# Optimization experiments

Hardware: AMD Instinct MI355X
Metric: run time of the kernel (lower is better)

Reference implementation:

```python
import jax, jax.numpy as jnp
import numpy as np

N_NODES = 100000
N_EDGES = 1600000
C = 256            # in_channels == out_channels
NUM_BUNDLES = 64
BUNDLE_DIM = 2
NUM_GRAPHS = 128
BN_EPS = 1e-5


def setup_inputs() -> dict:
    key = jax.random.key(0)
    ks = jax.random.split(key, 12)
    x = jax.random.normal(ks[0], (N_NODES, C), dtype=jnp.float32)
    edge_index = jax.random.randint(ks[1], (2, N_EDGES), 0, N_NODES, dtype=jnp.int64)
    batch = jnp.sort(jax.random.randint(ks[2], (N_NODES,), 0, NUM_GRAPHS, dtype=jnp.int64))
    s = 0.05
    # struct_enc MLP: Linear(C, 2*NB) -> GELU -> Linear(2*NB, NB)
    se_w1 = jax.random.normal(ks[3], (C, 2 * NUM_BUNDLES), dtype=jnp.float32) * s
    se_b1 = jnp.zeros((2 * NUM_BUNDLES,), dtype=jnp.float32)
    se_w2 = jax.random.normal(ks[4], (2 * NUM_BUNDLES, NUM_BUNDLES), dtype=jnp.float32) * s
    se_b2 = jnp.zeros((NUM_BUNDLES,), dtype=jnp.float32)
    # LimConv.lin: Linear(C, C)
    lin_w = jax.random.normal(ks[5], (C, C), dtype=jnp.float32) * s
    lin_b = jnp.zeros((C,), dtype=jnp.float32)
    # BatchNorm1d affine params
    bn_gamma = jnp.ones((C,), dtype=jnp.float32)
    bn_beta = jnp.zeros((C,), dtype=jnp.float32)
    return {"x": x, "edge_index": edge_index, "batch": batch,
            "se_w1": se_w1, "se_b1": se_b1, "se_w2": se_w2, "se_b2": se_b2,
            "lin_w": lin_w, "lin_b": lin_b, "bn_gamma": bn_gamma, "bn_beta": bn_beta}


def _lim_layer(x, batch, se_w1, se_b1, se_w2, se_b2, lin_w, lin_b, bn_gamma, bn_beta):
    n = x.shape[0]
    # vector field: [N, NB, 2, fiber]
    vf = x.reshape(n, NUM_BUNDLES, BUNDLE_DIM, -1)
    # struct_enc MLP -> per-bundle angle (tanh-squashed), euler map to SO(2)
    h1 = jax.nn.gelu(x @ se_w1 + se_b1, approximate=False)
    ang = jnp.tanh(h1 @ se_w2 + se_b2)          # [N, NB]
    c, s = jnp.cos(ang), jnp.sin(ang)
    # R[n,b] = [[c,-s],[s,c]]  -> [N, NB, 2, 2]
    rot = jnp.stack([jnp.stack([c, -s], axis=-1),
                     jnp.stack([s, c], axis=-1)], axis=-2)
    # rotate fibers
    vf = jnp.einsum('nbij,nbjf->nbif', rot, vf)
    h = vf.reshape(n, C) @ lin_w + lin_b
    # global mean pool over graphs, then broadcast back to nodes
    sums = jax.ops.segment_sum(h, batch, num_segments=NUM_GRAPHS)
    cnts = jax.ops.segment_sum(jnp.ones((n,), h.dtype), batch, num_segments=NUM_GRAPHS)
    hmean = sums / jnp.maximum(cnts, 1.0)[:, None]
    h = hmean[batch]
    # inverse rotation (R^T)
    vf = h.reshape(n, NUM_BUNDLES, BUNDLE_DIM, -1)
    vf = jnp.einsum('nbji,nbjf->nbif', rot, vf)
    h = vf.reshape(n, C)
    # residual (dim_in == dim_out)
    h = x + h
    # dropout p=0 / eval -> identity. BatchNorm1d with batch statistics.
    mu = jnp.mean(h, axis=0)
    var = jnp.var(h, axis=0)
    h = (h - mu) * jax.lax.rsqrt(var + BN_EPS) * bn_gamma + bn_beta
    return h


def reference(x, edge_index, batch, se_w1, se_b1, se_w2, se_b2, lin_w, lin_b, bn_gamma, bn_beta):
    # edge_index is unused when num_gnn == 0 (struct_enc is an MLP), as in the source.
    del edge_index
    return _lim_layer(x, batch, se_w1, se_b1, se_w2, se_b2, lin_w, lin_b, bn_gamma, bn_beta)
```

## Files before the change

### kernel.cpp

```cpp
#include <hip/hip_runtime.h>
#include <hip/hip_bf16.h>
#include <math.h>

#define N_NODES 100000
#define C 256
#define NB 64
#define H1D 128
#define NG 128
#define BN_EPS 1e-5f

#define BLKN 32
#define NSUB (N_NODES / BLKN)
#define NPART NSUB
#define WPB 4
#define NBLK1 ((NSUB + WPB - 1) / WPB)

#define GREC 769

#define OFF_GSUMS 0
#define OFF_BNSUM (NG * GREC)
#define OFF_BNSQ  (OFF_BNSUM + 256)
#define ZERO_FLOATS (OFF_BNSQ + 256)
#define OFF_HMEAN ZERO_FLOATS
#define OFF_WT1   (OFF_HMEAN + NG * C)
#define OFF_WT2   (OFF_WT1 + 16896)
#define OFF_CSN   (OFF_WT2 + 4352)
#define OFF_PBN   (OFF_CSN + N_NODES * 64)

#define WT1_LD 264
#define WT2_LD 136

typedef __attribute__((ext_vector_type(8))) short bf16x8;
typedef __attribute__((ext_vector_type(4))) float f32x4;

__device__ __forceinline__ float bf2f(__hip_bfloat16 h) { return __bfloat162float(h); }

__device__ __forceinline__ float fast_tanh(float y) {
    float e = __expf(2.f * y);
    return 1.f - 2.f / (e + 1.f);
}
__device__ __forceinline__ float fast_gelu(float v) {
    float u = 0.7978845608f * (v + 0.044715f * v * v * v);
    return 0.5f * v * (1.f + fast_tanh(u));
}

__device__ __forceinline__ bf16x8 pack8(float4 a, float4 b) {
    union { bf16x8 v; __hip_bfloat16 h[8]; } u;
    u.h[0] = __float2bfloat16(a.x); u.h[1] = __float2bfloat16(a.y);
    u.h[2] = __float2bfloat16(a.z); u.h[3] = __float2bfloat16(a.w);
    u.h[4] = __float2bfloat16(b.x); u.h[5] = __float2bfloat16(b.y);
    u.h[6] = __float2bfloat16(b.z); u.h[7] = __float2bfloat16(b.w);
    return u.v;
}

__global__ __launch_bounds__(256)
void k0_prep(const float* __restrict__ W1, const float* __restrict__ W2,
             float* __restrict__ ws,
             __hip_bfloat16* __restrict__ Wt1, __hip_bfloat16* __restrict__ Wt2)
{
    const int t0 = threadIdx.x + blockIdx.x * 256;
    const int stride = gridDim.x * 256;
    for (int i = t0; i < ZERO_FLOATS; i += stride)
        ws[i] = 0.f;
    for (int i = t0; i < 128 * 256; i += stride) {
        int n = i >> 8, k = i & 255;
        Wt1[n * WT1_LD + k] = __float2bfloat16(W1[k * 128 + n]);
    }
    for (int i = t0; i < 64 * 128; i += stride) {
        int n = i >> 7, k = i & 127;
        Wt2[n * WT2_LD + k] = __float2bfloat16(W2[k * 64 + n]);
    }
}

__global__ __launch_bounds__(256, 4)
void k1_wave(const float* __restrict__ x,
             const int* __restrict__ batch,
             const __hip_bfloat16* __restrict__ Wt1g,
             const float* __restrict__ b1,
             const __hip_bfloat16* __restrict__ Wt2g,
             const float* __restrict__ b2,
             float* __restrict__ gsums,
             float* __restrict__ pbn,
             __hip_bfloat16* __restrict__ csng)
{
    __shared__ __hip_bfloat16 h1s4[WPB][BLKN][WT2_LD];
    __shared__ int gsh4[WPB][BLKN];

    const int t = threadIdx.x;
    const int wv = t >> 6;
    const int l = t & 63;
    const int lo = l & 15, quad = l >> 4;
    const int wid = blockIdx.x * WPB + wv;
    if (wid >= NSUB) return;
    const int n0 = wid * BLKN;

    auto h1s = h1s4[wv];
    auto csn = (__hip_bfloat16 (*)[132])&h1s4[wv][0][0];
    int* gsh = gsh4[wv];

    if (l < BLKN) gsh[l] = batch[n0 + l];

    f32x4 acc1[2][8];
    #pragma unroll
    for (int nt = 0; nt < 8; ++nt) { acc1[0][nt] = (f32x4)0.f; acc1[1][nt] = (f32x4)0.f; }

    const float* xr0 = x + (size_t)(n0 + lo) * C + quad * 8;
    const short* w1row = (const short*)Wt1g + lo * WT1_LD + quad * 8;
    #pragma unroll
    for (int k = 0; k < 8; ++k) {
        float4 u00 = *(const float4*)(xr0 + k * 32);
        float4 u01 = *(const float4*)(xr0 + k * 32 + 4);
        float4 u10 = *(const float4*)(xr0 + 16 * C + k * 32);
        float4 u11 = *(const float4*)(xr0 + 16 * C + k * 32 + 4);
        bf16x8 a0 = pack8(u00, u01);
        bf16x8 a1 = pack8(u10, u11);
        #pragma unroll
        for (int nt = 0; nt < 8; ++nt) {
            bf16x8 bB = *(const bf16x8*)(w1row + nt * 16 * WT1_LD + k * 32);
            acc1[0][nt] = __builtin_amdgcn_mfma_f32_16x16x32_bf16(a0, bB, acc1[0][nt], 0, 0, 0);
            acc1[1][nt] = __builtin_amdgcn_mfma_f32_16x16x32_bf16(a1, bB, acc1[1][nt], 0, 0, 0);
        }
    }

    #pragma unroll
    for (int nt = 0; nt < 8; ++nt) {
        const float bb = b1[nt * 16 + lo];
        #pragma unroll
        for (int mt = 0; mt < 2; ++mt) {
            #pragma unroll
            for (int r = 0; r < 4; ++r) {
                float v = fast_gelu(acc1[mt][nt][r] + bb);
                h1s[mt * 16 + quad * 4 + r][nt * 16 + lo] = __float2bfloat16(v);
            }
        }
    }

    f32x4 acc2[2][4];
    #pragma unroll
    for (int nt = 0; nt < 4; ++nt) { acc2[0][nt] = (f32x4)0.f; acc2[1][nt] = (f32x4)0.f; }
    const short* w2row = (const short*)Wt2g + lo * WT2_LD + quad * 8;
    #pragma unroll
    for (int k = 0; k < 4; ++k) {
        bf16x8 af0 = *(const bf16x8*)&h1s[lo][k * 32 + quad * 8];
        bf16x8 af1 = *(const bf16x8*)&h1s[16 + lo][k * 32 + quad * 8];
        #pragma unroll
        for (int nt = 0; nt < 4; ++nt) {
            bf16x8 bB = *(const bf16x8*)(w2row + nt * 16 * WT2_LD + k * 32);
            acc2[0][nt] = __builtin_amdgcn_mfma_f32_16x16x32_bf16(af0, bB, acc2[0][nt], 0, 0, 0);
            acc2[1][nt] = __builtin_amdgcn_mfma_f32_16x16x32_bf16(af1, bB, acc2[1][nt], 0, 0, 0);
        }
    }

    #pragma unroll
    for (int nt = 0; nt < 4; ++nt) {
        const int col = nt * 16 + lo;
        const float bb = b2[col];
        #pragma unroll
        for (int mt = 0; mt < 2; ++mt) {
            #pragma unroll
            for (int r = 0; r < 4; ++r) {
                float a = fast_tanh(acc2[mt][nt][r] + bb);
                union { unsigned int u; __hip_bfloat16 h[2]; } p;
                p.h[0] = __float2bfloat16(__cosf(a));
                p.h[1] = __float2bfloat16(__sinf(a));
                *(unsigned int*)&csn[mt * 16 + quad * 4 + r][2 * col] = p.u;
            }
        }
    }

    #pragma unroll
    for (int m = 0; m < 16; ++m) {
        int idx = l + m * 64;
        int row = idx >> 5;
        int q = idx & 31;
        uint2 v = *(const uint2*)&csn[row][q * 4];
        *(uint2*)(csng + (size_t)(n0 + row) * 128 + q * 4) = v;
    }

    const int c0 = 4 * l;
    float xc0 = 0.f, xc1 = 0.f, xc2 = 0.f, xc3 = 0.f;
    float xs0 = 0.f, xs1 = 0.f, xs2 = 0.f, xs3 = 0.f;
    float xm0 = 0.f, xm1 = 0.f, xm2 = 0.f, xm3 = 0.f;
    float xq0 = 0.f, xq1 = 0.f, xq2 = 0.f, xq3 = 0.f;
    float stc = 0.f, sts = 0.f, stcc = 0.f, stcs = 0.f, rcnt = 0.f;
    int gprev = -1;

#define FLUSH_G(gidx) do {                                            \
        float* rec = gsums + (size_t)(gidx) * GREC;                   \
        atomicAdd(&rec[c0 + 0], xc0); atomicAdd(&rec[c0 + 1], xc1);   \
        atomicAdd(&rec[c0 + 2], xc2); atomicAdd(&rec[c0 + 3], xc3);   \
        atomicAdd(&rec[256 + c0 + 0], xs0); atomicAdd(&rec[256 + c0 + 1], xs1); \
        atomicAdd(&rec[256 + c0 + 2], xs2); atomicAdd(&rec[256 + c0 + 3], xs3); \
        atomicAdd(&rec[512 + c0 + 0], stc); atomicAdd(&rec[512 + c0 + 1], sts); \
        atomicAdd(&rec[512 + c0 + 2], stcc); atomicAdd(&rec[512 + c0 + 3], stcs); \
        if (l == 0) atomicAdd(&rec[768], rcnt);                       \
    } while (0)

    #pragma unroll 8
    for (int r = 0; r < BLKN; ++r) {
        const int g = gsh[r];
        if (g != gprev) {
            if (gprev >= 0) FLUSH_G(gprev);
            xc0 = xc1 = xc2 = xc3 = 0.f;
            xs0 = xs1 = xs2 = xs3 = 0.f;
            stc = sts = stcc = stcs = 0.f;
            rcnt = 0.f;
            gprev = g;
        }
        const float4 xv = *(const float4*)(x + (size_t)(n0 + r) * C + c0);
        union { unsigned int u; __hip_bfloat16 h[2]; } cs;
        cs.u = *(const unsigned int*)&csn[r][2 * l];
        const float cv = bf2f(cs.h[0]);
        const float sv = bf2f(cs.h[1]);
        xc0 += xv.x * cv; xc1 += xv.y * cv; xc2 += xv.z * cv; xc3 += xv.w * cv;
        xs0 += xv.x * sv; xs1 += xv.y * sv; xs2 += xv.z * sv; xs3 += xv.w * sv;
        xm0 += xv.x; xm1 += xv.y; xm2 += xv.z; xm3 += xv.w;
        xq0 += xv.x * xv.x; xq1 += xv.y * xv.y; xq2 += xv.z * xv.z; xq3 += xv.w * xv.w;
        stc += cv; sts += sv; stcc += cv * cv; stcs += cv * sv;
        rcnt += 1.f;
    }
    if (gprev >= 0) FLUSH_G(gprev);
#undef FLUSH_G

    float4 m4; m4.x = xm0; m4.y = xm1; m4.z = xm2; m4.w = xm3;
    float4 q4; q4.x = xq0; q4.y = xq1; q4.z = xq2; q4.w = xq3;
    *(float4*)&pbn[(size_t)wid * 512 + c0] = m4;
    *(float4*)&pbn[(size_t)wid * 512 + 256 + c0] = q4;
}

__global__ __launch_bounds__(256)
void k2_hmean_stats(const float* __restrict__ gsums,
                    const float* __restrict__ pbn,
                    const float* __restrict__ lin_w, const float* __restrict__ lin_b,
                    float* __restrict__ hmean,
                    float* __restrict__ bnsum, float* __restrict__ bnsq)
{
    __shared__ float xc[C], xsv[C], bs4[C], grot[C], hm[C];
    __shared__ float cnt_sh;
    const int g = blockIdx.x;
    const int t = threadIdx.x;

    {
        const int chunk = (NPART + NG - 1) / NG;
        const int r0 = g * chunk;
        const int r1 = (r0 + chunk < NPART) ? (r0 + chunk) : NPART;
        if (r0 < r1) {
            float a0 = 0.f, a1 = 0.f;
            for (int r = r0; r < r1; ++r) {
                a0 += pbn[(size_t)r * 512 + t];
                a1 += pbn[(size_t)r * 512 + 256 + t];
            }
            atomicAdd(&bnsum[t], a0);
            atomicAdd(&bnsq[t], a1);
        }
    }

    const float* rec = gsums + (size_t)g * GREC;
    xc[t]  = rec[t];
    xsv[t] = rec[256 + t];
    bs4[t] = rec[512 + t];
    if (t == 0) cnt_sh = rec[768];
    __syncthreads();

    const int b = t >> 2, idx2 = t & 3, i2 = idx2 >> 1;
    grot[t] = (i2 == 0) ? (xc[t] - xsv[t + 2]) : (xsv[t - 2] + xc[t]);
    __syncthreads();

    float a0 = 0.f, a1 = 0.f, a2 = 0.f, a3 = 0.f;
    #pragma unroll 4
    for (int k = 0; k < C; k += 4) {
        a0 += grot[k + 0] * lin_w[(size_t)(k + 0) * C + t];
        a1 += grot[k + 1] * lin_w[(size_t)(k + 1) * C + t];
        a2 += grot[k + 2] * lin_w[(size_t)(k + 2) * C + t];
        a3 += grot[k + 3] * lin_w[(size_t)(k + 3) * C + t];
    }
    const float cnt = cnt_sh;
    const float hv = (cnt > 0.f) ? ((a0 + a1 + a2 + a3) / cnt + lin_b[t]) : 0.f;
    hm[t] = hv;
    hmean[g * C + t] = hv;
    __syncthreads();

    if (cnt > 0.f) {
        const int f = idx2 & 1;
        const float h0 = hm[4 * b + f];
        const float h1 = hm[4 * b + 2 + f];
        const float CV = bs4[4 * b + 0], SV = bs4[4 * b + 1];
        const float CC = bs4[4 * b + 2], CS = bs4[4 * b + 3];
        const float SS = cnt - CC;
        float sumc, sqc;
        if (i2 == 0) {
            sumc = h0 * CV + h1 * SV;
            sqc  = 2.f * (h0 * xc[t] + h1 * xsv[t])
                 + h0 * h0 * CC + 2.f * h0 * h1 * CS + h1 * h1 * SS;
        } else {
            sumc = -h0 * SV + h1 * CV;
            sqc  = 2.f * (-h0 * xsv[t] + h1 * xc[t])
                 + h0 * h0 * SS - 2.f * h0 * h1 * CS + h1 * h1 * CC;
        }
        atomicAdd(&bnsum[t], sumc);
        atomicAdd(&bnsq[t], sqc);
    }
}

__global__ __launch_bounds__(256, 4)
void k4_fused(const float* __restrict__ x,
              const int* __restrict__ batch,
              const __hip_bfloat16* __restrict__ csng,
              const float* __restrict__ hmean,
              const float* __restrict__ bnsum, const float* __restrict__ bnsq,
              const float* __restrict__ gamma, const float* __restrict__ beta,
              float* __restrict__ out)
{
    __shared__ float mul_s[C], add_s[C];
    const int t = threadIdx.x;
    {
        const float inv_n = 1.0f / (float)N_NODES;
        const float mu = bnsum[t] * inv_n;
        const float var = bnsq[t] * inv_n - mu * mu;
        const float inv = rsqrtf(var + BN_EPS);
        const float m = gamma[t] * inv;
        mul_s[t] = m;
        add_s[t] = beta[t] - mu * m;
    }
    __syncthreads();
    const int s = t >> 6;
    const int cg4 = t & 63;
    const float4 mm = *(const float4*)&mul_s[cg4 * 4];
    const float4 aa = *(const float4*)&add_s[cg4 * 4];

    for (int base = blockIdx.x * 4; base < N_NODES; base += gridDim.x * 4) {
        const int n = base + s;
        if (n < N_NODES) {
            const int g = batch[n];
            const float4 hm = *(const float4*)(hmean + (size_t)g * C + cg4 * 4);
            union { unsigned int u; __hip_bfloat16 h[2]; } cs;
            cs.u = *(const unsigned int*)(csng + (size_t)n * 128 + cg4 * 2);
            const float cv = bf2f(cs.h[0]);
            const float sv = bf2f(cs.h[1]);
            const float4 xv = *(const float4*)(x + (size_t)n * C + cg4 * 4);
            float4 o;
            o.x = (xv.x + cv * hm.x + sv * hm.z) * mm.x + aa.x;
            o.y = (xv.y + cv * hm.y + sv * hm.w) * mm.y + aa.y;
            o.z = (xv.z - sv * hm.x + cv * hm.z) * mm.z + aa.z;
            o.w = (xv.w - sv * hm.y + cv * hm.w) * mm.w + aa.w;
            *(float4*)(out + (size_t)n * C + cg4 * 4) = o;
        }
    }
}

extern "C" void kernel_launch(void* const* d_in, const int* in_sizes, int n_in,
                              void* d_out, int out_size, void* d_ws, size_t ws_size,
                              hipStream_t stream)
{
    const float* x      = (const float*)d_in[0];
    const int* batch    = (const int*)d_in[2];
    const float* W1     = (const float*)d_in[3];
    const float* b1     = (const float*)d_in[4];
    const float* W2     = (const float*)d_in[5];
    const float* b2     = (const float*)d_in[6];
    const float* lin_w  = (const float*)d_in[7];
    const float* lin_b  = (const float*)d_in[8];
    const float* gamma  = (const float*)d_in[9];
    const float* beta   = (const float*)d_in[10];

    float* ws    = (float*)d_ws;
    float* gsums = ws + OFF_GSUMS;
    float* bnsum = ws + OFF_BNSUM;
    float* bnsq  = ws + OFF_BNSQ;
    float* hmean = ws + OFF_HMEAN;
    __hip_bfloat16* Wt1  = (__hip_bfloat16*)(ws + OFF_WT1);
    __hip_bfloat16* Wt2  = (__hip_bfloat16*)(ws + OFF_WT2);
    __hip_bfloat16* csng = (__hip_bfloat16*)(ws + OFF_CSN);
    float* pbn   = ws + OFF_PBN;
    float* out   = (float*)d_out;

    k0_prep<<<512, 256, 0, stream>>>(W1, W2, ws, Wt1, Wt2);
    k1_wave<<<NBLK1, 256, 0, stream>>>(x, batch, Wt1, b1, Wt2, b2,
                                       gsums, pbn, csng);
    k2_hmean_stats<<<NG, 256, 0, stream>>>(gsums, pbn, lin_w, lin_b, hmean, bnsum, bnsq);
    k4_fused<<<2048, 256, 0, stream>>>(x, batch, csng, hmean, bnsum, bnsq,
                                       gamma, beta, out);
}
```

Baseline: 315.5 us.

## Halve per-wave node tile and pre-reduce BN partials per block

Each wave in the MLP/statistics kernel now handles 16 nodes instead of 32, and blocks hold 2 waves (128 threads) instead of 4. This gives more waves for latency hiding and lowers register use. The per-wave BatchNorm partial sums are combined in shared memory before one store per block, which halves the partial count that the next kernel must reduce. In exchange, each wave reuses the loaded weight tiles over fewer rows, so weight traffic per node rises, and each block now needs a __syncthreads.

Measured after the change: 353.5 us. 12.1% more time.

```diff
diff --git a/kernel.cpp b/kernel.cpp
--- a/kernel.cpp
+++ b/kernel.cpp
@@ -9,11 +9,11 @@
 #define NG 128
 #define BN_EPS 1e-5f
 
-#define BLKN 32
+#define BLKN 16
 #define NSUB (N_NODES / BLKN)
-#define NPART NSUB
-#define WPB 4
-#define NBLK1 ((NSUB + WPB - 1) / WPB)
+#define WPB 2
+#define NBLK1 (NSUB / WPB)
+#define NPART NBLK1
 
 #define GREC 769
 
@@ -72,7 +72,7 @@
     }
 }
 
-__global__ __launch_bounds__(256, 4)
+__global__ __launch_bounds__(128, 6)
 void k1_wave(const float* __restrict__ x,
              const int* __restrict__ batch,
              const __hip_bfloat16* __restrict__ Wt1g,
@@ -83,26 +83,26 @@
              float* __restrict__ pbn,
              __hip_bfloat16* __restrict__ csng)
 {
-    __shared__ __hip_bfloat16 h1s4[WPB][BLKN][WT2_LD];
-    __shared__ int gsh4[WPB][BLKN];
+    __shared__ __hip_bfloat16 h1s2[WPB][BLKN][WT2_LD];
+    __shared__ int gsh2[WPB][BLKN];
+    __shared__ float pbs[WPB][512];
 
     const int t = threadIdx.x;
     const int wv = t >> 6;
     const int l = t & 63;
     const int lo = l & 15, quad = l >> 4;
     const int wid = blockIdx.x * WPB + wv;
-    if (wid >= NSUB) return;
     const int n0 = wid * BLKN;
 
-    auto h1s = h1s4[wv];
-    auto csn = (__hip_bfloat16 (*)[132])&h1s4[wv][0][0];
-    int* gsh = gsh4[wv];
+    auto h1s = h1s2[wv];
+    auto csn = (__hip_bfloat16 (*)[132])&h1s2[wv][0][0];
+    int* gsh = gsh2[wv];
 
     if (l < BLKN) gsh[l] = batch[n0 + l];
 
-    f32x4 acc1[2][8];
-    #pragma unroll
-    for (int nt = 0; nt < 8; ++nt) { acc1[0][nt] = (f32x4)0.f; acc1[1][nt] = (f32x4)0.f; }
+    f32x4 acc1[8];
+    #pragma unroll
+    for (int nt = 0; nt < 8; ++nt) acc1[nt] = (f32x4)0.f;
 
     const float* xr0 = x + (size_t)(n0 + lo) * C + quad * 8;
     const short* w1row = (const short*)Wt1g + lo * WT1_LD + quad * 8;
@@ -110,15 +110,11 @@
     for (int k = 0; k < 8; ++k) {
         float4 u00 = *(const float4*)(xr0 + k * 32);
         float4 u01 = *(const float4*)(xr0 + k * 32 + 4);
-        float4 u10 = *(const float4*)(xr0 + 16 * C + k * 32);
-        float4 u11 = *(const float4*)(xr0 + 16 * C + k * 32 + 4);
         bf16x8 a0 = pack8(u00, u01);
-        bf16x8 a1 = pack8(u10, u11);
         #pragma unroll
         for (int nt = 0; nt < 8; ++nt) {
             bf16x8 bB = *(const bf16x8*)(w1row + nt * 16 * WT1_LD + k * 32);
-            acc1[0][nt] = __builtin_amdgcn_mfma_f32_16x16x32_bf16(a0, bB, acc1[0][nt], 0, 0, 0);
-            acc1[1][nt] = __builtin_amdgcn_mfma_f32_16x16x32_bf16(a1, bB, acc1[1][nt], 0, 0, 0);
+            acc1[nt] = __builtin_amdgcn_mfma_f32_16x16x32_bf16(a0, bB, acc1[nt], 0, 0, 0);
         }
     }
 
@@ -126,28 +122,23 @@
     for (int nt = 0; nt < 8; ++nt) {
         const float bb = b1[nt * 16 + lo];
         #pragma unroll
-        for (int mt = 0; mt < 2; ++mt) {
-            #pragma unroll
-            for (int r = 0; r < 4; ++r) {
-                float v = fast_gelu(acc1[mt][nt][r] + bb);
-                h1s[mt * 16 + quad * 4 + r][nt * 16 + lo] = __float2bfloat16(v);
-            }
-        }
-    }
-
-    f32x4 acc2[2][4];
-    #pragma unroll
-    for (int nt = 0; nt < 4; ++nt) { acc2[0][nt] = (f32x4)0.f; acc2[1][nt] = (f32x4)0.f; }
+        for (int r = 0; r < 4; ++r) {
+            float v = fast_gelu(acc1[nt][r] + bb);
+            h1s[quad * 4 + r][nt * 16 + lo] = __float2bfloat16(v);
+        }
+    }
+
+    f32x4 acc2[4];
+    #pragma unroll
+    for (int nt = 0; nt < 4; ++nt) acc2[nt] = (f32x4)0.f;
     const short* w2row = (const short*)Wt2g + lo * WT2_LD + quad * 8;
     #pragma unroll
     for (int k = 0; k < 4; ++k) {
         bf16x8 af0 = *(const bf16x8*)&h1s[lo][k * 32 + quad * 8];
-        bf16x8 af1 = *(const bf16x8*)&h1s[16 + lo][k * 32 + quad * 8];
         #pragma unroll
         for (int nt = 0; nt < 4; ++nt) {
             bf16x8 bB = *(const bf16x8*)(w2row + nt * 16 * WT2_LD + k * 32);
-            acc2[0][nt] = __builtin_amdgcn_mfma_f32_16x16x32_bf16(af0, bB, acc2[0][nt], 0, 0, 0);
-            acc2[1][nt] = __builtin_amdgcn_mfma_f32_16x16x32_bf16(af1, bB, acc2[1][nt], 0, 0, 0);
+            acc2[nt] = __builtin_amdgcn_mfma_f32_16x16x32_bf16(af0, bB, acc2[nt], 0, 0, 0);
         }
     }
 
@@ -156,20 +147,17 @@
         const int col = nt * 16 + lo;
         const float bb = b2[col];
         #pragma unroll
-        for (int mt = 0; mt < 2; ++mt) {
-            #pragma unroll
-            for (int r = 0; r < 4; ++r) {
-                float a = fast_tanh(acc2[mt][nt][r] + bb);
-                union { unsigned int u; __hip_bfloat16 h[2]; } p;
-                p.h[0] = __float2bfloat16(__cosf(a));
-                p.h[1] = __float2bfloat16(__sinf(a));
-                *(unsigned int*)&csn[mt * 16 + quad * 4 + r][2 * col] = p.u;
-            }
-        }
-    }
-
-    #pragma unroll
-    for (int m = 0; m < 16; ++m) {
+        for (int r = 0; r < 4; ++r) {
+            float a = fast_tanh(acc2[nt][r] + bb);
+            union { unsigned int u; __hip_bfloat16 h[2]; } p;
+            p.h[0] = __float2bfloat16(__cosf(a));
+            p.h[1] = __float2bfloat16(__sinf(a));
+            *(unsigned int*)&csn[quad * 4 + r][2 * col] = p.u;
+        }
+    }
+
+    #pragma unroll
+    for (int m = 0; m < 8; ++m) {
         int idx = l + m * 64;
         int row = idx >> 5;
         int q = idx & 31;
@@ -222,10 +210,22 @@
     if (gprev >= 0) FLUSH_G(gprev);
 #undef FLUSH_G
 
-    float4 m4; m4.x = xm0; m4.y = xm1; m4.z = xm2; m4.w = xm3;
-    float4 q4; q4.x = xq0; q4.y = xq1; q4.z = xq2; q4.w = xq3;
-    *(float4*)&pbn[(size_t)wid * 512 + c0] = m4;
-    *(float4*)&pbn[(size_t)wid * 512 + 256 + c0] = q4;
+    {
+        float4 m4; m4.x = xm0; m4.y = xm1; m4.z = xm2; m4.w = xm3;
+        float4 q4; q4.x = xq0; q4.y = xq1; q4.z = xq2; q4.w = xq3;
+        *(float4*)&pbs[wv][c0] = m4;
+        *(float4*)&pbs[wv][256 + c0] = q4;
+    }
+    __syncthreads();
+    {
+        const int i4 = 4 * t;
+        float4 s0 = *(const float4*)&pbs[0][i4];
+        float4 s1 = *(const float4*)&pbs[1][i4];
+        float4 o;
+        o.x = s0.x + s1.x; o.y = s0.y + s1.y;
+        o.z = s0.z + s1.z; o.w = s0.w + s1.w;
+        *(float4*)&pbn[(size_t)blockIdx.x * 512 + i4] = o;
+    }
 }
 
 __global__ __launch_bounds__(256)
@@ -375,7 +375,7 @@
     float* out   = (float*)d_out;
 
     k0_prep<<<512, 256, 0, stream>>>(W1, W2, ws, Wt1, Wt2);
-    k1_wave<<<NBLK1, 256, 0, stream>>>(x, batch, Wt1, b1, Wt2, b2,
+    k1_wave<<<NBLK1, 128, 0, stream>>>(x, batch, Wt1, b1, Wt2, b2,
                                        gsums, pbn, csng);
     k2_hmean_stats<<<NG, 256, 0, stream>>>(gsums, pbn, lin_w, lin_b, hmean, bnsum, bnsq);
     k4_fused<<<2048, 256, 0, stream>>>(x, batch, csng, hmean, bnsum, bnsq,
```
